# Kernel tuning notes

Hardware: AMD Instinct MI355X
Metric: run time of the kernel (lower is better)

Reference implementation:

```python
import jax, jax.numpy as jnp
import numpy as np

N = 100_000      # nodes
E = 800_000      # edges per edge type
T = 3            # num_edge_types - 1 relation-specific convs
D_IN = 128
D_OUT = 128


def setup_inputs() -> dict:
    key = jax.random.key(0)
    k1, k2, k3, k4 = jax.random.split(key, 4)
    x = jax.random.normal(k1, (N, D_IN), dtype=jnp.float32)
    edges = jax.random.randint(k2, (T, 2, E), 0, N, dtype=jnp.int32)
    W = jax.random.normal(k3, (T, D_IN, D_OUT), dtype=jnp.float32) * (1.0 / np.sqrt(D_IN))
    b = jax.random.normal(k4, (T, D_OUT), dtype=jnp.float32) * 0.02
    return {"x": x, "edges": edges, "W": W, "b": b}


def _gcn_conv(x, ei, W, b):
    """PyG GCNConv: add self-loops, symmetric D^-1/2 (A+I) D^-1/2 norm, XW, +b."""
    n = x.shape[0]
    xw = x @ W                                   # [N, D_OUT]
    loop = jnp.arange(n, dtype=ei.dtype)
    src = jnp.concatenate([ei[0], loop])         # [E+N]
    dst = jnp.concatenate([ei[1], loop])         # [E+N]
    deg = jax.ops.segment_sum(jnp.ones(src.shape[0], xw.dtype), dst, num_segments=n)
    dis = jnp.where(deg > 0, jax.lax.rsqrt(jnp.maximum(deg, 1e-12)), 0.0)
    norm = dis[src] * dis[dst]                   # [E+N]
    msg = xw[src] * norm[:, None]                # gather-transform: [E+N, D_OUT]
    out = jax.ops.segment_sum(msg, dst, num_segments=n)  # scatter-add back to nodes
    return out + b


def reference(x, edges, W, b):
    # Sum of per-edge-type GCN convolutions into a shared output buffer.
    out = jnp.zeros((x.shape[0], W.shape[-1]), dtype=x.dtype)
    for i in range(edges.shape[0]):              # small fixed relation loop
        out = out + _gcn_conv(x, edges[i], W[i], b[i])
    return out
```

## Files before the change

kernel.cpp:

```cpp
#include <hip/hip_runtime.h>

#define NN 100000
#define EE 800000
#define TT 3
#define D  128
#define NB 391
#define CAPB 7168
#define CHUNK 8192
#define LSTRIDE 392
#define CAP 64
#define ENC 8191.0f

typedef unsigned short bf16_t;

typedef __bf16 bf16x8_t __attribute__((ext_vector_type(8)));
typedef float  f32x4_t  __attribute__((ext_vector_type(4)));

union ABFrag { bf16x8_t v; uint4 q; };

__device__ __forceinline__ bf16_t f2bf(float f) {
    unsigned u = __float_as_uint(f);
    u += 0x7fff + ((u >> 16) & 1);
    return (bf16_t)(u >> 16);
}
__device__ __forceinline__ float bf_lo(unsigned p) { return __uint_as_float(p << 16); }
__device__ __forceinline__ float bf_hi(unsigned p) { return __uint_as_float(p & 0xFFFF0000u); }

__global__ void quant_kernel(const float* __restrict__ x, bf16_t* __restrict__ xq) {
    int i = (blockIdx.x * 256 + threadIdx.x) * 4;
    if (i >= NN * D) return;
    float4 f = *(const float4*)(x + i);
    uint2 p;
    p.x = (unsigned)f2bf(f.x) | ((unsigned)f2bf(f.y) << 16);
    p.y = (unsigned)f2bf(f.z) | ((unsigned)f2bf(f.w) << 16);
    *(uint2*)(xq + i) = p;
}

__global__ __launch_bounds__(512, 8) void bin_kernel(const int* __restrict__ edges,
                                                     int* __restrict__ bcnt,
                                                     unsigned* __restrict__ bin) {
    __shared__ int hist[NB];
    __shared__ int lbase[NB];
    __shared__ int gbase[NB];
    __shared__ int scn[512];
    __shared__ unsigned srec[CHUNK];
    int tid = threadIdx.x;
    int t = blockIdx.y;
    int f0 = blockIdx.x * CHUNK;
    const int* sb = edges + (size_t)t * 2 * EE;
    const int* db = sb + EE;

    for (int i = tid; i < NB; i += 512) hist[i] = 0;
    __syncthreads();

    int4 s4[4], d4[4];
    int rnk[16];
    bool have[4];
#pragma unroll
    for (int j = 0; j < 4; ++j) {
        int e = f0 + ((j * 512 + tid) << 2);
        have[j] = (e < EE);
        if (have[j]) { s4[j] = *(const int4*)(sb + e); d4[j] = *(const int4*)(db + e); }
    }
#pragma unroll
    for (int j = 0; j < 4; ++j) {
        if (have[j]) {
            rnk[j * 4 + 0] = atomicAdd(&hist[d4[j].x >> 8], 1);
            rnk[j * 4 + 1] = atomicAdd(&hist[d4[j].y >> 8], 1);
            rnk[j * 4 + 2] = atomicAdd(&hist[d4[j].z >> 8], 1);
            rnk[j * 4 + 3] = atomicAdd(&hist[d4[j].w >> 8], 1);
        }
    }
    __syncthreads();

    int hv = (tid < NB) ? hist[tid] : 0;
    scn[tid] = hv;
    __syncthreads();
    for (int off = 1; off < 512; off <<= 1) {
        int u = 0;
        if (tid >= off) u = scn[tid - off];
        __syncthreads();
        if (tid >= off) scn[tid] += u;
        __syncthreads();
    }
    if (tid < NB) {
        lbase[tid] = scn[tid] - hv;
        gbase[tid] = (hv > 0) ? atomicAdd(&bcnt[tid], hv) : 0;
    }
    __syncthreads();

#pragma unroll
    for (int j = 0; j < 4; ++j) {
        if (have[j]) {
            int ss[4] = {s4[j].x, s4[j].y, s4[j].z, s4[j].w};
            int dd[4] = {d4[j].x, d4[j].y, d4[j].z, d4[j].w};
#pragma unroll
            for (int k = 0; k < 4; ++k) {
                int bkt = dd[k] >> 8;
                int pos = lbase[bkt] + rnk[j * 4 + k];
                srec[pos] = ((unsigned)(dd[k] & 255) << 19) | ((unsigned)t << 17) | (unsigned)ss[k];
            }
        }
    }
    __syncthreads();

    int nval = EE - f0; if (nval > CHUNK) nval = CHUNK;
    for (int i = tid; i < nval; i += 512) {
        int lo = 0;
#pragma unroll
        for (int step = 256; step > 0; step >>= 1) {
            int cand = lo + step;
            if (cand < NB && lbase[cand] <= i) lo = cand;
        }
        int rel = gbase[lo] + (i - lbase[lo]);
        if (rel < CAPB) bin[(size_t)lo * CAPB + rel] = srec[i];
    }
}

#define MAXR 14
__global__ __launch_bounds__(512) void count_kernel(const int* __restrict__ bcnt,
                                                    const unsigned* __restrict__ bin,
                                                    float* __restrict__ dis3,
                                                    int* __restrict__ cnts3,
                                                    const float* __restrict__ W,
                                                    bf16_t* __restrict__ WT) {
    int tid = threadIdx.x;
    int b = blockIdx.x;
    if (b >= NB) {
        int t = b - NB;
        for (int i = tid; i < D * D; i += 512) {
            int n = i >> 7, k = i & 127;
            WT[((size_t)t * D + n) * D + k] = f2bf(W[((size_t)t * D + k) * D + n]);
        }
        return;
    }
    __shared__ int cnt[768];
    int c = bcnt[b]; if (c > CAPB) c = CAPB;
    const unsigned* reg = bin + (size_t)b * CAPB;

    for (int i = tid; i < 768; i += 512) cnt[i] = 0;
    __syncthreads();
#pragma unroll
    for (int k = 0; k < MAXR; ++k) {
        int i = tid + k * 512;
        if (i < c) {
            unsigned u = reg[i];
            atomicAdd(&cnt[(int)(u >> 19) * 3 + (int)((u >> 17) & 3)], 1);
        }
    }
    __syncthreads();
    if (tid < 256) {
        int gnode = b * 256 + tid;
        if (gnode < NN) {
            int d0 = cnt[tid * 3], d1 = cnt[tid * 3 + 1], d2 = cnt[tid * 3 + 2];
            cnts3[gnode]         = d0 | (d1 << 8) | (d2 << 16);
            dis3[gnode]          = rsqrtf((float)d0 + 1.f);
            dis3[NN + gnode]     = rsqrtf((float)d1 + 1.f);
            dis3[2 * NN + gnode] = rsqrtf((float)d2 + 1.f);
        }
    }
}

__global__ __launch_bounds__(512) void slot_kernel(const int* __restrict__ bcnt,
                                                   const unsigned* __restrict__ bin,
                                                   const float* __restrict__ dis3,
                                                   const int* __restrict__ cnts3,
                                                   unsigned* __restrict__ recs) {
    __shared__ int rkc[256];
    __shared__ float dnl[3][256];
    int tid = threadIdx.x;
    int b = blockIdx.x;
    int c = bcnt[b]; if (c > CAPB) c = CAPB;
    const unsigned* reg = bin + (size_t)b * CAPB;
    unsigned* base = recs + (size_t)b * 256 * CAP;

    if (tid < 256) {
        int gnode = b * 256 + tid;
        int pk = (gnode < NN) ? cnts3[gnode] : 0;
        dnl[0][tid] = rsqrtf((float)(pk & 255) + 1.f);
        dnl[1][tid] = rsqrtf((float)((pk >> 8) & 255) + 1.f);
        dnl[2][tid] = rsqrtf((float)((pk >> 16) & 255) + 1.f);
        rkc[tid] = 0;
    }
    for (int i = tid; i < 256 * CAP; i += 512) base[i] = 0u;
    __syncthreads();

#pragma unroll
    for (int k = 0; k < MAXR; ++k) {
        int i = tid + k * 512;
        if (i < c) {
            unsigned u = reg[i];
            int node8 = (int)(u >> 19);
            int t = (int)((u >> 17) & 3);
            int src = (int)(u & 0x1FFFFu);
            float w = dis3[t * NN + src] * dnl[t][node8];
            int r = atomicAdd(&rkc[node8], 1);
            if (r < CAP)
                base[node8 * CAP + r] =
                    ((unsigned)(w * ENC + 0.5f) << 19) | ((unsigned)t << 17) | (unsigned)src;
        }
    }
}


#define ISSUE(UX, SA, UW, J0)                                                      \
    {                                                                              \
        const int _j0 = (J0);                                                      \
        _Pragma("unroll")                                                          \
        for (int k = 0; k < 8; ++k) {                                              \
            SA[k] = __builtin_amdgcn_readlane((int)(UW), _j0 + k);                 \
            int sxk = SA[k] & 0x1FFFF;                                             \
            UX[k] = *(const unsigned*)(xq + (size_t)sxk * D + (lane << 1));        \
        }                                                                          \
    }

#define CONSUME(UX, SA, A00, A01, A10, A11, A20, A21)                              \
    {                                                                              \
        _Pragma("unroll")                                                          \
        for (int k = 0; k < 8; ++k) {                                              \
            unsigned sa = (unsigned)SA[k];                                         \
            float wk = (float)(sa >> 19);                                          \
            int tk = (int)((sa >> 17) & 3);                                        \
            unsigned u = UX[k];                                                    \
            float xl = bf_lo(u), xh = bf_hi(u);                                    \
            if (tk == 0)      { A00 += wk * xl; A01 += wk * xh; }                  \
            else if (tk == 1) { A10 += wk * xl; A11 += wk * xh; }                  \
            else              { A20 += wk * xl; A21 += wk * xh; }                  \
        }                                                                          \
    }

__global__ __launch_bounds__(512, 8) void fused_kernel(const bf16_t* __restrict__ xq,
                                                       const int* __restrict__ cnts3,
                                                       const unsigned* __restrict__ recs,
                                                       const bf16_t* __restrict__ WT,
                                                       const float* __restrict__ bias,
                                                       float* __restrict__ out) {
    __shared__ __attribute__((aligned(16))) ushort ylds[16 * LSTRIDE];
    int tid  = threadIdx.x;
    int lane = tid & 63;
    int wave = tid >> 6;
    int n0 = blockIdx.x * 16;
    int nA = n0 + wave * 2;
    int nB = nA + 1;

    unsigned uwA = recs[(size_t)nA * CAP + lane];
    unsigned uwB = recs[(size_t)nB * CAP + lane];
    unsigned suA = *(const unsigned*)(xq + (size_t)nA * D + (lane << 1));
    unsigned suB = *(const unsigned*)(xq + (size_t)nB * D + (lane << 1));
    int pkA = cnts3[nA], pkB = cnts3[nB];

    int dA0 = pkA & 255, dA1 = (pkA >> 8) & 255, dA2 = (pkA >> 16) & 255;
    int dB0 = pkB & 255, dB1 = (pkB >> 8) & 255, dB2 = (pkB >> 16) & 255;
    float dnA0 = rsqrtf((float)dA0 + 1.f), dnA1 = rsqrtf((float)dA1 + 1.f),
          dnA2 = rsqrtf((float)dA2 + 1.f);
    float dnB0 = rsqrtf((float)dB0 + 1.f), dnB1 = rsqrtf((float)dB1 + 1.f),
          dnB2 = rsqrtf((float)dB2 + 1.f);
    int cTA = dA0 + dA1 + dA2; if (cTA > CAP) cTA = CAP;
    int cTB = dB0 + dB1 + dB2; if (cTB > CAP) cTB = CAP;
    int cSA = __builtin_amdgcn_readfirstlane(cTA);
    int cSB = __builtin_amdgcn_readfirstlane(cTB);

    float xsA0 = bf_lo(suA), xsA1 = bf_hi(suA);
    float xsB0 = bf_lo(suB), xsB1 = bf_hi(suB);

    float aA00 = dnA0 * dnA0 * ENC * xsA0, aA01 = dnA0 * dnA0 * ENC * xsA1;
    float aA10 = dnA1 * dnA1 * ENC * xsA0, aA11 = dnA1 * dnA1 * ENC * xsA1;
    float aA20 = dnA2 * dnA2 * ENC * xsA0, aA21 = dnA2 * dnA2 * ENC * xsA1;
    float aB00 = dnB0 * dnB0 * ENC * xsB0, aB01 = dnB0 * dnB0 * ENC * xsB1;
    float aB10 = dnB1 * dnB1 * ENC * xsB0, aB11 = dnB1 * dnB1 * ENC * xsB1;
    float aB20 = dnB2 * dnB2 * ENC * xsB0, aB21 = dnB2 * dnB2 * ENC * xsB1;

    unsigned uxA[8], uxB[8];
    int sA[8], sB[8];

    int nbA = (cSA + 7) >> 3;
    int nbB = (cSB + 7) >> 3;
    if (nbA > 0) ISSUE(uxA, sA, uwA, 0)
    if (nbB > 0) ISSUE(uxB, sB, uwB, 0)
    int nbmax = nbA > nbB ? nbA : nbB;
    for (int blk = 0; blk < nbmax; ++blk) {
        if (blk < nbA) {
            CONSUME(uxA, sA, aA00, aA01, aA10, aA11, aA20, aA21)
            if (blk + 1 < nbA) ISSUE(uxA, sA, uwA, (blk + 1) * 8)
        }
        if (blk < nbB) {
            CONSUME(uxB, sB, aB00, aB01, aB10, aB11, aB20, aB21)
            if (blk + 1 < nbB) ISSUE(uxB, sB, uwB, (blk + 1) * 8)
        }
    }

    {
        const float fs = 1.0f / ENC;
        ushort* ywA = ylds + (wave * 2) * LSTRIDE + (lane << 1);
        ushort* ywB = ywA + LSTRIDE;
        *(unsigned*)(ywA)         = (unsigned)f2bf(aA00 * fs) | ((unsigned)f2bf(aA01 * fs) << 16);
        *(unsigned*)(ywA + D)     = (unsigned)f2bf(aA10 * fs) | ((unsigned)f2bf(aA11 * fs) << 16);
        *(unsigned*)(ywA + 2 * D) = (unsigned)f2bf(aA20 * fs) | ((unsigned)f2bf(aA21 * fs) << 16);
        *(unsigned*)(ywB)         = (unsigned)f2bf(aB00 * fs) | ((unsigned)f2bf(aB01 * fs) << 16);
        *(unsigned*)(ywB + D)     = (unsigned)f2bf(aB10 * fs) | ((unsigned)f2bf(aB11 * fs) << 16);
        *(unsigned*)(ywB + 2 * D) = (unsigned)f2bf(aB20 * fs) | ((unsigned)f2bf(aB21 * fs) << 16);
    }
    __syncthreads();

    {
        int quad = lane >> 4;
        int lid  = lane & 15;
        int col  = wave * 16 + lid;
        f32x4_t acc = {0.f, 0.f, 0.f, 0.f};
        const ushort* yr = ylds + lid * LSTRIDE;
#pragma unroll
        for (int t = 0; t < TT; ++t) {
            const bf16_t* wn = WT + ((size_t)t * D + col) * D;
#pragma unroll
            for (int s = 0; s < 4; ++s) {
                ABFrag av, bv;
                av.q = *(const uint4*)(yr + t * D + s * 32 + quad * 8);
                bv.q = *(const uint4*)(wn + s * 32 + quad * 8);
                acc = __builtin_amdgcn_mfma_f32_16x16x32_bf16(av.v, bv.v, acc, 0, 0, 0);
            }
        }
        float bc = bias[col] + bias[D + col] + bias[2 * D + col];
#pragma unroll
        for (int r = 0; r < 4; ++r)
            out[(size_t)(n0 + quad * 4 + r) * D + col] = acc[r] + bc;
    }
}

extern "C" void kernel_launch(void* const* d_in, const int* in_sizes, int n_in,
                              void* d_out, int out_size, void* d_ws, size_t ws_size,
                              hipStream_t stream) {
    const float* x     = (const float*)d_in[0];
    const int*   edges = (const int*)d_in[1];
    const float* W     = (const float*)d_in[2];
    const float* b     = (const float*)d_in[3];
    float*       out   = (float*)d_out;

    char* w = (char*)d_ws;
    bf16_t*   xq    = (bf16_t*)w;
    unsigned* bin   = (unsigned*)(w + (size_t)NN * D * 2);
    unsigned* recs  = (unsigned*)((char*)bin + (size_t)NB * CAPB * 4);
    float*    dis3  = (float*)((char*)recs + (size_t)NB * 256 * CAP * 4);
    int*      cnts3 = (int*)((char*)dis3 + (size_t)3 * NN * 4);
    bf16_t*   WT    = (bf16_t*)(cnts3 + NN);
    int*      bcnt  = (int*)((char*)WT + (size_t)TT * D * D * 2);

    hipMemsetAsync(bcnt, 0, (size_t)NB * sizeof(int), stream);

    quant_kernel<<<(NN * D / 4 + 255) / 256, 256, 0, stream>>>(x, xq);

    {
        dim3 g((EE + CHUNK - 1) / CHUNK, TT);
        bin_kernel<<<g, 512, 0, stream>>>(edges, bcnt, bin);
    }

    count_kernel<<<NB + TT, 512, 0, stream>>>(bcnt, bin, dis3, cnts3, W, WT);

    slot_kernel<<<NB, 512, 0, stream>>>(bcnt, bin, dis3, cnts3, recs);

    fused_kernel<<<NN / 16, 512, 0, stream>>>(xq, cnts3, recs, WT, b, out);
}
```

Baseline: 318.3 us.

## Deepen gather prefetch to three stages, precompute bin targets, drop record zeroing

```diff
diff --git a/kernel.cpp b/kernel.cpp
--- a/kernel.cpp
+++ b/kernel.cpp
@@ -36,7 +36,7 @@
     *(uint2*)(xq + i) = p;
 }
 
-__global__ __launch_bounds__(512, 8) void bin_kernel(const int* __restrict__ edges,
+__global__ __launch_bounds__(512, 4) void bin_kernel(const int* __restrict__ edges,
                                                      int* __restrict__ bcnt,
                                                      unsigned* __restrict__ bin) {
     __shared__ int hist[NB];
@@ -44,6 +44,7 @@
     __shared__ int gbase[NB];
     __shared__ int scn[512];
     __shared__ unsigned srec[CHUNK];
+    __shared__ unsigned stgt[CHUNK];
     int tid = threadIdx.x;
     int t = blockIdx.y;
     int f0 = blockIdx.x * CHUNK;
@@ -97,8 +98,11 @@
 #pragma unroll
             for (int k = 0; k < 4; ++k) {
                 int bkt = dd[k] >> 8;
-                int pos = lbase[bkt] + rnk[j * 4 + k];
+                int r = rnk[j * 4 + k];
+                int pos = lbase[bkt] + r;
+                int rel = gbase[bkt] + r;
                 srec[pos] = ((unsigned)(dd[k] & 255) << 19) | ((unsigned)t << 17) | (unsigned)ss[k];
+                stgt[pos] = (rel < CAPB) ? (unsigned)(bkt * CAPB + rel) : 0xFFFFFFFFu;
             }
         }
     }
@@ -106,14 +110,8 @@
 
     int nval = EE - f0; if (nval > CHUNK) nval = CHUNK;
     for (int i = tid; i < nval; i += 512) {
-        int lo = 0;
-#pragma unroll
-        for (int step = 256; step > 0; step >>= 1) {
-            int cand = lo + step;
-            if (cand < NB && lbase[cand] <= i) lo = cand;
-        }
-        int rel = gbase[lo] + (i - lbase[lo]);
-        if (rel < CAPB) bin[(size_t)lo * CAPB + rel] = srec[i];
+        unsigned tg = stgt[i];
+        if (tg != 0xFFFFFFFFu) bin[tg] = srec[i];
     }
 }
 
@@ -182,7 +180,6 @@
         dnl[2][tid] = rsqrtf((float)((pk >> 16) & 255) + 1.f);
         rkc[tid] = 0;
     }
-    for (int i = tid; i < 256 * CAP; i += 512) base[i] = 0u;
     __syncthreads();
 
 #pragma unroll
@@ -203,12 +200,13 @@
 }
 
 
-#define ISSUE(UX, SA, UW, J0)                                                      \
+#define ISSUE(UX, SA, UW, J0, CS)                                                  \
     {                                                                              \
         const int _j0 = (J0);                                                      \
         _Pragma("unroll")                                                          \
         for (int k = 0; k < 8; ++k) {                                              \
-            SA[k] = __builtin_amdgcn_readlane((int)(UW), _j0 + k);                 \
+            int rl = __builtin_amdgcn_readlane((int)(UW), _j0 + k);                \
+            SA[k] = ((_j0 + k) < (CS)) ? rl : 0;    \
             int sxk = SA[k] & 0x1FFFF;                                             \
             UX[k] = *(const unsigned*)(xq + (size_t)sxk * D + (lane << 1));        \
         }                                                                          \
@@ -229,7 +227,18 @@
         }                                                                          \
     }
 
-__global__ __launch_bounds__(512, 8) void fused_kernel(const bf16_t* __restrict__ xq,
+#define STEP_A(UX, SA, OFF)                                                        \
+    if (blk + (OFF) < nbA) {                                                       \
+        CONSUME(UX, SA, aA00, aA01, aA10, aA11, aA20, aA21)                        \
+        if (blk + (OFF) + 3 < nbA) ISSUE(UX, SA, uwA, (blk + (OFF) + 3) * 8, cSA)  \
+    }
+#define STEP_B(UX, SA, OFF)                                                        \
+    if (blk + (OFF) < nbB) {                                                       \
+        CONSUME(UX, SA, aB00, aB01, aB10, aB11, aB20, aB21)                        \
+        if (blk + (OFF) + 3 < nbB) ISSUE(UX, SA, uwB, (blk + (OFF) + 3) * 8, cSB)  \
+    }
+
+__global__ __launch_bounds__(512, 7) void fused_kernel(const bf16_t* __restrict__ xq,
                                                        const int* __restrict__ cnts3,
                                                        const unsigned* __restrict__ recs,
                                                        const bf16_t* __restrict__ WT,
@@ -270,23 +279,27 @@
     float aB10 = dnB1 * dnB1 * ENC * xsB0, aB11 = dnB1 * dnB1 * ENC * xsB1;
     float aB20 = dnB2 * dnB2 * ENC * xsB0, aB21 = dnB2 * dnB2 * ENC * xsB1;
 
-    unsigned uxA[8], uxB[8];
-    int sA[8], sB[8];
+    unsigned uxA0[8], uxA1[8], uxA2[8], uxB0[8], uxB1[8], uxB2[8];
+    int sA0[8], sA1[8], sA2[8], sB0[8], sB1[8], sB2[8];
 
     int nbA = (cSA + 7) >> 3;
     int nbB = (cSB + 7) >> 3;
-    if (nbA > 0) ISSUE(uxA, sA, uwA, 0)
-    if (nbB > 0) ISSUE(uxB, sB, uwB, 0)
+
+    if (nbA > 0) ISSUE(uxA0, sA0, uwA, 0, cSA)
+    if (nbB > 0) ISSUE(uxB0, sB0, uwB, 0, cSB)
+    if (nbA > 1) ISSUE(uxA1, sA1, uwA, 8, cSA)
+    if (nbB > 1) ISSUE(uxB1, sB1, uwB, 8, cSB)
+    if (nbA > 2) ISSUE(uxA2, sA2, uwA, 16, cSA)
+    if (nbB > 2) ISSUE(uxB2, sB2, uwB, 16, cSB)
+
     int nbmax = nbA > nbB ? nbA : nbB;
-    for (int blk = 0; blk < nbmax; ++blk) {
-        if (blk < nbA) {
-            CONSUME(uxA, sA, aA00, aA01, aA10, aA11, aA20, aA21)
-            if (blk + 1 < nbA) ISSUE(uxA, sA, uwA, (blk + 1) * 8)
-        }
-        if (blk < nbB) {
-            CONSUME(uxB, sB, aB00, aB01, aB10, aB11, aB20, aB21)
-            if (blk + 1 < nbB) ISSUE(uxB, sB, uwB, (blk + 1) * 8)
-        }
+    for (int blk = 0; blk < nbmax; blk += 3) {
+        STEP_A(uxA0, sA0, 0)
+        STEP_B(uxB0, sB0, 0)
+        STEP_A(uxA1, sA1, 1)
+        STEP_B(uxB1, sB1, 1)
+        STEP_A(uxA2, sA2, 2)
+        STEP_B(uxB2, sB2, 2)
     }
 
     {
```

Measured after the change: 349.7 us. +9.9%, slower.
